# Kernel tuning notes

Measured on AMD Instinct MI355X. Metric: run time of the kernel, lower is better.

## Reference

```python
import jax, jax.numpy as jnp
import numpy as np

LOG2PI = float(np.log(2.0 * np.pi))


def setup_inputs() -> dict:
    key = jax.random.key(0)
    ks = jax.random.split(key, 5)
    B, T, XD, C = 128, 2050, 6, 64
    return {
        "x": jax.random.normal(ks[0], (B, T, XD), jnp.float32),
        "observation_means": jax.random.uniform(ks[1], (C, XD), dtype=jnp.float32),
        "observation_stddevs": jax.random.uniform(ks[2], (C, XD), dtype=jnp.float32),
        "log_A": jax.random.normal(ks[3], (C, C), jnp.float32),
        "log_pi": jax.random.normal(ks[4], (C,), jnp.float32),
    }


def _emission_logprob(x, means, stds):
    # Normal(means[:, :4], relu(stds[:, :4]) + 0.1).log_prob(x[:, :, :4]) summed over feat dim
    mu = means[:, :4]                       # (C,4)
    sigma = jax.nn.relu(stds[:, :4]) + 0.1  # (C,4)
    z = (x[:, :, None, :4] - mu) / sigma    # (B,T,C,4)
    return jnp.sum(-0.5 * z * z - jnp.log(sigma) - 0.5 * LOG2PI, axis=-1)  # (B,T,C)


def _forward_scalers(logp, log_A, log_pi):
    # scaled HMM forward pass; returns per-step log normalizers (T,B)
    a0 = logp[:, 0] + log_pi
    s0 = jax.nn.logsumexp(a0, axis=-1)
    a0n = a0 - s0[:, None]

    def step(a_prev, lp_t):
        a = lp_t + jax.nn.logsumexp(a_prev[:, :, None] + log_A[None], axis=1)
        s = jax.nn.logsumexp(a, axis=-1)
        return a - s[:, None], s

    _, s_rest = jax.lax.scan(step, a0n, jnp.swapaxes(logp[:, 1:], 0, 1))
    return jnp.concatenate([s0[None], s_rest], axis=0)  # (T,B)


def _viterbi(logp, log_A, log_pi):
    d0 = logp[:, 0] + log_pi  # (B,C)

    def step(d_prev, lp_t):
        scores = d_prev[:, :, None] + log_A[None]  # (B,C_prev,C_cur)
        psi_t = jnp.argmax(scores, axis=1)
        d = jnp.max(scores, axis=1) + lp_t
        return d, psi_t

    d_last, psi = jax.lax.scan(step, d0, jnp.swapaxes(logp[:, 1:], 0, 1))  # psi: (T-1,B,C)
    c_last = jnp.argmax(d_last, axis=-1)  # (B,)

    def back(c_next, psi_t):
        c_t = jnp.take_along_axis(psi_t, c_next[:, None], axis=1)[:, 0]
        return c_t, c_t

    _, cs = jax.lax.scan(back, c_last, psi, reverse=True)  # (T-1,B)
    c = jnp.concatenate([cs, c_last[None]], axis=0)  # (T,B)
    return jnp.swapaxes(c, 0, 1)  # (B,T)


def reference(x, observation_means, observation_stddevs, log_A, log_pi):
    logA = jax.nn.log_softmax(log_A, axis=1)
    logpi = jax.nn.log_softmax(log_pi, axis=0)
    logp = _emission_logprob(x, observation_means, observation_stddevs)  # (B,T,C)
    scalers = _forward_scalers(logp, logA, logpi)                         # (T,B)
    logp_x = jnp.sum(scalers, axis=0)                                     # (B,)
    c_est = _viterbi(logp, logA, logpi)                                   # (B,T) int
    return logp_x, c_est
```

## Files before the change

### kernel.cpp

```cpp
#include <hip/hip_runtime.h>

#define T_LEN 2050
#define B_SZ 128
#define NCHUNK 33
#define HL2PI 0.91893853320467274178f

__device__ __forceinline__ float waveMax(float v) {
#pragma unroll
    for (int off = 32; off >= 1; off >>= 1)
        v = fmaxf(v, __shfl_xor(v, off, 64));
    return v;
}
__device__ __forceinline__ float waveSum(float v) {
#pragma unroll
    for (int off = 32; off >= 1; off >>= 1)
        v += __shfl_xor(v, off, 64);
    return v;
}
__device__ __forceinline__ void waveArgmax(float& v, int& idx) {
#pragma unroll
    for (int off = 32; off >= 1; off >>= 1) {
        float ov = __shfl_xor(v, off, 64);
        int   oi = __shfl_xor(idx, off, 64);
        if (ov > v || (ov == v && oi < idx)) { v = ov; idx = oi; }
    }
}
__device__ __forceinline__ void cfence() { asm volatile("" ::: "memory"); }

__device__ __forceinline__ float rl(float v, int lane) {
    return __int_as_float(__builtin_amdgcn_readlane(__float_as_int(v), lane));
}

__device__ __forceinline__ float dppSumAll(float v) {
#define SSTEP(ctrl) { int t_ = __builtin_amdgcn_update_dpp(0, __float_as_int(v), ctrl, 0xf, 0xf, true); \
                      v = v + __int_as_float(t_); }
    SSTEP(0x111) SSTEP(0x112) SSTEP(0x114) SSTEP(0x118) SSTEP(0x142) SSTEP(0x143)
#undef SSTEP
    return __int_as_float(__builtin_amdgcn_readlane(__float_as_int(v), 63));
}
__device__ __forceinline__ float dppMaxAll(float v) {
#define MSTEP(ctrl) { int t_ = __builtin_amdgcn_update_dpp(__float_as_int(v), __float_as_int(v), ctrl, 0xf, 0xf, false); \
                      v = fmaxf(v, __int_as_float(t_)); }
    MSTEP(0x111) MSTEP(0x112) MSTEP(0x114) MSTEP(0x118) MSTEP(0x142) MSTEP(0x143)
#undef MSTEP
    return __int_as_float(__builtin_amdgcn_readlane(__float_as_int(v), 63));
}

extern "C" __global__ __launch_bounds__(64, 1)
void hmm_prep(const float* __restrict__ logA_in,
              const float* __restrict__ logpi_in,
              float* __restrict__ lAg,
              float* __restrict__ lpig)
{
    __shared__ float la[64 * 65];
    __shared__ float rowlse[64];
    const int j = threadIdx.x;
#pragma unroll
    for (int k = 0; k < 64; ++k)
        la[k * 65 + j] = logA_in[k * 64 + j];
    cfence();
    {
        float m = -1e30f;
#pragma unroll
        for (int k = 0; k < 64; ++k) m = fmaxf(m, la[j * 65 + k]);
        float s = 0.f;
#pragma unroll
        for (int k = 0; k < 64; ++k) s += expf(la[j * 65 + k] - m);
        rowlse[j] = m + logf(s);
    }
    cfence();
    {
        float v = logpi_in[j];
        float m = waveMax(v);
        float s = waveSum(expf(v - m));
        lpig[j] = v - (m + logf(s));
    }
    float4* o = (float4*)lAg;
#pragma unroll
    for (int k = 0; k < 16; ++k) {
        float4 v;
        v.x = la[(4 * k + 0) * 65 + j] - rowlse[4 * k + 0];
        v.y = la[(4 * k + 1) * 65 + j] - rowlse[4 * k + 1];
        v.z = la[(4 * k + 2) * 65 + j] - rowlse[4 * k + 2];
        v.w = la[(4 * k + 3) * 65 + j] - rowlse[4 * k + 3];
        o[j * 16 + k] = v;
    }
}

extern "C" __global__ __launch_bounds__(256)
void hmm_emis(const float* __restrict__ x,
              const float* __restrict__ means,
              const float* __restrict__ stds,
              float* __restrict__ buf,
              float* __restrict__ m_pre)
{
    const int wid = blockIdx.x * 4 + (threadIdx.x >> 6);
    const int j = threadIdx.x & 63;
    const int t = wid >> 7;
    const int b = wid & 127;

    const float* xt = x + ((size_t)b * T_LEN + t) * 6;
    float x0 = xt[0], x1 = xt[1], x2 = xt[2], x3 = xt[3];

    float mu0 = means[j * 6 + 0], mu1 = means[j * 6 + 1];
    float mu2 = means[j * 6 + 2], mu3 = means[j * 6 + 3];
    float sg0 = fmaxf(stds[j * 6 + 0], 0.f) + 0.1f;
    float sg1 = fmaxf(stds[j * 6 + 1], 0.f) + 0.1f;
    float sg2 = fmaxf(stds[j * 6 + 2], 0.f) + 0.1f;
    float sg3 = fmaxf(stds[j * 6 + 3], 0.f) + 0.1f;
    float ls0 = logf(sg0), ls1 = logf(sg1), ls2 = logf(sg2), ls3 = logf(sg3);

    float z0 = (x0 - mu0) / sg0, z1 = (x1 - mu1) / sg1;
    float z2 = (x2 - mu2) / sg2, z3 = (x3 - mu3) / sg3;
    float e0 = ((-0.5f * z0) * z0 - ls0) - HL2PI;
    float e1 = ((-0.5f * z1) * z1 - ls1) - HL2PI;
    float e2 = ((-0.5f * z2) * z2 - ls2) - HL2PI;
    float e3 = ((-0.5f * z3) * z3 - ls3) - HL2PI;
    float lp = ((e0 + e1) + e2) + e3;

    buf[((size_t)b * T_LEN + t) * 64 + j] = lp;
    float mm = waveMax(lp);
    if (j == 0) m_pre[(size_t)b * T_LEN + t] = mm;
}

extern "C" __global__ __launch_bounds__(64, 1)
void hmm_main(const float* __restrict__ x,
              const float* __restrict__ means,
              const float* __restrict__ stds,
              const float* __restrict__ lAg,
              const float* __restrict__ lpig,
              float* __restrict__ out,
              float* __restrict__ buf,
              const float* __restrict__ m_pre,
              int* __restrict__ c_last)
{
    __shared__ __align__(16) float xs[12304];

    const int j   = threadIdx.x;
    const int bid = blockIdx.x;
    const bool is_fwd = (bid < B_SZ);
    const int b = is_fwd ? bid : bid - B_SZ;

    float lpi = lpig[j];

    if (is_fwd) {
        {
            const float4* xg4 = (const float4*)(x + (size_t)b * T_LEN * 6);
            float4* xs4 = (float4*)xs;
            for (int i = j; i < 3075; i += 64) xs4[i] = xg4[i];
        }
        float mu0 = means[j * 6 + 0], mu1 = means[j * 6 + 1];
        float mu2 = means[j * 6 + 2], mu3 = means[j * 6 + 3];
        float sg0 = fmaxf(stds[j * 6 + 0], 0.f) + 0.1f;
        float sg1 = fmaxf(stds[j * 6 + 1], 0.f) + 0.1f;
        float sg2 = fmaxf(stds[j * 6 + 2], 0.f) + 0.1f;
        float sg3 = fmaxf(stds[j * 6 + 3], 0.f) + 0.1f;
        float ls0 = logf(sg0), ls1 = logf(sg1), ls2 = logf(sg2), ls3 = logf(sg3);
        float i0 = 1.f / sg0, i1 = 1.f / sg1, i2 = 1.f / sg2, i3 = 1.f / sg3;
        float cst = -(ls0 + ls1 + ls2 + ls3) - 4.f * HL2PI;

        float Ac[64];
        {
            const float4* g = (const float4*)lAg;
#pragma unroll
            for (int k = 0; k < 16; ++k) {
                float4 v = g[j * 16 + k];
                Ac[4 * k + 0] = __expf(v.x); Ac[4 * k + 1] = __expf(v.y);
                Ac[4 * k + 2] = __expf(v.z); Ac[4 * k + 3] = __expf(v.w);
            }
        }
        cfence();

        float z0 = (xs[0] - mu0) * i0, z1 = (xs[1] - mu1) * i1;
        float z2 = (xs[2] - mu2) * i2, z3 = (xs[3] - mu3) * i3;
        float a0 = (cst - 0.5f * (z0 * z0 + z1 * z1 + z2 * z2 + z3 * z3)) + lpi;
        float m0a = dppMaxAll(a0);
        float u = __expf(a0 - m0a);
        float s0 = dppSumAll(u);
        double acc = (double)(m0a + __logf(s0));
        u *= (1.0f / s0);

        const float* mp = m_pre + (size_t)b * T_LEN;
        float g0 = mp[1], g1 = mp[2], g2 = mp[3], g3 = mp[4];

#pragma unroll 1
        for (int t = 1; t < T_LEN; ++t) {
            float mm_c = g0; g0 = g1; g1 = g2; g2 = g3;
            int tp = t + 4; if (tp > T_LEN - 1) tp = T_LEN - 1;
            g3 = mp[tp];

            int o = t * 6;
            float y0 = xs[o], y1 = xs[o + 1], y2 = xs[o + 2], y3 = xs[o + 3];
            float w0 = (y0 - mu0) * i0, w1 = (y1 - mu1) * i1;
            float w2 = (y2 - mu2) * i2, w3 = (y3 - mu3) * i3;
            float lp = cst - 0.5f * (w0 * w0 + w1 * w1 + w2 * w2 + w3 * w3);
            float e_c = __expf(lp - mm_c);

            float q0 = 0.f, q1 = 0.f, q2 = 0.f, q3 = 0.f;
#pragma unroll
            for (int gq = 0; gq < 4; ++gq) {
                float s[16];
#pragma unroll
                for (int m = 0; m < 16; ++m) s[m] = rl(u, 16 * gq + m);
#pragma unroll
                for (int k2 = 0; k2 < 4; ++k2) {
                    const int i = 16 * gq + 4 * k2;
                    q0 = fmaf(s[4 * k2 + 0], Ac[i + 0], q0);
                    q1 = fmaf(s[4 * k2 + 1], Ac[i + 1], q1);
                    q2 = fmaf(s[4 * k2 + 2], Ac[i + 2], q2);
                    q3 = fmaf(s[4 * k2 + 3], Ac[i + 3], q3);
                }
            }
            u = ((q0 + q1) + (q2 + q3)) * e_c;
            acc += (double)mm_c;
            if ((t & 3) == 0) {
                float ss = dppSumAll(u);
                acc += (double)__logf(ss);
                u *= (1.0f / ss);
            }
        }
        float sf = dppSumAll(u);
        acc += (double)__logf(sf);
        if (j == 0) out[b] = (float)acc;
    } else {
        float lA[64];
        {
            const float4* g = (const float4*)lAg;
#pragma unroll
            for (int k = 0; k < 16; ++k) {
                float4 v = g[j * 16 + k];
                lA[4 * k + 0] = v.x; lA[4 * k + 1] = v.y;
                lA[4 * k + 2] = v.z; lA[4 * k + 3] = v.w;
            }
        }
        float* bb = buf + (size_t)b * T_LEN * 64 + j;

        float dn = bb[0] + lpi;
        float l0 = bb[64], l1 = bb[128], l2 = bb[192], l3 = bb[256];
        bb[0] = dn;

#pragma unroll 1
        for (int t = 1; t < T_LEN; ++t) {
            float lp_c = l0; l0 = l1; l1 = l2; l2 = l3;
            int tp = t + 4; if (tp > T_LEN - 1) tp = T_LEN - 1;
            l3 = bb[(size_t)tp * 64];

            float m0 = -3.4e38f, m1 = -3.4e38f, m2 = -3.4e38f, m3 = -3.4e38f;
#pragma unroll
            for (int gq = 0; gq < 4; ++gq) {
                float s[16];
#pragma unroll
                for (int m = 0; m < 16; ++m) s[m] = rl(dn, 16 * gq + m);
#pragma unroll
                for (int k2 = 0; k2 < 4; k2 += 2) {
                    const int ia = 16 * gq + 4 * k2;
                    const int ib = ia + 4;
                    float a0_ = s[4 * k2 + 0] + lA[ia + 0], b0_ = s[4 * k2 + 4] + lA[ib + 0];
                    float a1_ = s[4 * k2 + 1] + lA[ia + 1], b1_ = s[4 * k2 + 5] + lA[ib + 1];
                    float a2_ = s[4 * k2 + 2] + lA[ia + 2], b2_ = s[4 * k2 + 6] + lA[ib + 2];
                    float a3_ = s[4 * k2 + 3] + lA[ia + 3], b3_ = s[4 * k2 + 7] + lA[ib + 3];
                    m0 = fmaxf(fmaxf(m0, a0_), b0_);
                    m1 = fmaxf(fmaxf(m1, a1_), b1_);
                    m2 = fmaxf(fmaxf(m2, a2_), b2_);
                    m3 = fmaxf(fmaxf(m3, a3_), b3_);
                }
            }
            dn = fmaxf(fmaxf(m0, m1), fmaxf(m2, m3)) + lp_c;

            bb[(size_t)t * 64] = dn;
        }

        float vv = dn; int idx = j;
        waveArgmax(vv, idx);
        if (j == 0) c_last[b] = idx;
    }
}

extern "C" __global__ __launch_bounds__(256)
void hmm_psi(const float* __restrict__ buf,
             const float* __restrict__ lAg,
             unsigned char* __restrict__ psi)
{
    __shared__ __align__(16) float sd[4][64];
    const int warp = threadIdx.x >> 6;
    const int j = threadIdx.x & 63;
    const int wid = blockIdx.x * 4 + warp;

    float lA[64];
    {
        const float4* g = (const float4*)lAg;
#pragma unroll
        for (int k = 0; k < 16; ++k) {
            float4 v = g[j * 16 + k];
            lA[4 * k + 0] = v.x; lA[4 * k + 1] = v.y;
            lA[4 * k + 2] = v.z; lA[4 * k + 3] = v.w;
        }
    }
    const float4* dv = (const float4*)sd[warp];
    const int NP = 2049 * B_SZ;

    for (int p = wid; p < NP; p += 8192) {
        const int t = (p >> 7) + 1;
        const int b = p & 127;
        float dval = buf[((size_t)b * T_LEN + (t - 1)) * 64 + j];
        sd[warp][j] = dval;

        float bv0 = -3.4e38f, bv1 = -3.4e38f, bv2 = -3.4e38f, bv3 = -3.4e38f;
        int bi0 = 0, bi1 = 1, bi2 = 2, bi3 = 3;
#pragma unroll
        for (int k = 0; k < 16; ++k) {
            float4 dd = dv[k];
            float v0 = dd.x + lA[4 * k + 0];
            float v1 = dd.y + lA[4 * k + 1];
            float v2 = dd.z + lA[4 * k + 2];
            float v3 = dd.w + lA[4 * k + 3];
            if (v0 > bv0) { bv0 = v0; bi0 = 4 * k + 0; }
            if (v1 > bv1) { bv1 = v1; bi1 = 4 * k + 1; }
            if (v2 > bv2) { bv2 = v2; bi2 = 4 * k + 2; }
            if (v3 > bv3) { bv3 = v3; bi3 = 4 * k + 3; }
        }
        float best = bv0; int bidx = bi0;
        if (bv1 > best || (bv1 == best && bi1 < bidx)) { best = bv1; bidx = bi1; }
        if (bv2 > best || (bv2 == best && bi2 < bidx)) { best = bv2; bidx = bi2; }
        if (bv3 > best || (bv3 == best && bi3 < bidx)) { best = bv3; bidx = bi3; }

        psi[((size_t)t * B_SZ + b) * 64 + j] = (unsigned char)bidx;
    }
}

extern "C" __global__ __launch_bounds__(256)
void hmm_compose(const unsigned char* __restrict__ psi,
                 unsigned char* __restrict__ mt)
{
    const int w = blockIdx.x * 4 + (threadIdx.x >> 6);
    const int j = threadIdx.x & 63;
    const int g = w % NCHUNK;
    const int b = w / NCHUNK;
    const int e = (g < NCHUNK - 1) ? g * 64 + 64 : (T_LEN - 1);
    int M = j;
    for (int t = e; t >= g * 64 + 1; --t)
        M = psi[((size_t)t * B_SZ + b) * 64 + M];
    mt[((size_t)g * B_SZ + b) * 64 + j] = (unsigned char)M;
}

extern "C" __global__ __launch_bounds__(64, 1)
void hmm_fill(const unsigned char* __restrict__ psi,
              const unsigned char* __restrict__ mt,
              const int* __restrict__ c_last,
              float* __restrict__ out)
{
    __shared__ int sb[NCHUNK];
    const int b = blockIdx.x;
    const int g = threadIdx.x;
    const int cl = c_last[b];
    if (g == 0) {
        int cur = cl;
        for (int q = NCHUNK - 1; q >= 0; --q) {
            cur = mt[((size_t)q * B_SZ + b) * 64 + cur];
            sb[q] = cur;
        }
    }
    cfence();
    float* oc = out + B_SZ + (size_t)b * T_LEN;
    if (g == NCHUNK) {
        oc[T_LEN - 1] = (float)cl;
    } else if (g < NCHUNK) {
        const int e = (g < NCHUNK - 1) ? g * 64 + 64 : (T_LEN - 1);
        int s = (g < NCHUNK - 1) ? sb[g + 1] : cl;
        for (int t = e; t >= g * 64 + 1; --t) {
            s = psi[((size_t)t * B_SZ + b) * 64 + s];
            oc[t - 1] = (float)s;
        }
    }
}

extern "C" void kernel_launch(void* const* d_in, const int* in_sizes, int n_in,
                              void* d_out, int out_size, void* d_ws, size_t ws_size,
                              hipStream_t stream)
{
    const float* x      = (const float*)d_in[0];
    const float* means  = (const float*)d_in[1];
    const float* stds   = (const float*)d_in[2];
    const float* logA   = (const float*)d_in[3];
    const float* logpi  = (const float*)d_in[4];
    float* out = (float*)d_out;

    char* base = (char*)d_ws;
    float*         buf   = (float*)base;
    unsigned char* psi   = (unsigned char*)(base + 67174400);
    float*         m_pre = (float*)(base + 67174400);
    unsigned char* mt    = (unsigned char*)(base + 83968000);
    int*           cl    = (int*)(base + 84238336);
    float*         lAg   = (float*)(base + 84238848);
    float*         lpig  = (float*)(base + 84255232);

    hipLaunchKernelGGL(hmm_prep, dim3(1), dim3(64), 0, stream, logA, logpi, lAg, lpig);
    hipLaunchKernelGGL(hmm_emis, dim3((T_LEN * B_SZ) / 4), dim3(256), 0, stream,
                       x, means, stds, buf, m_pre);
    hipLaunchKernelGGL(hmm_main, dim3(2 * B_SZ), dim3(64), 0, stream,
                       x, means, stds, lAg, lpig, out, buf, m_pre, cl);
    hipLaunchKernelGGL(hmm_psi, dim3(2048), dim3(256), 0, stream, buf, lAg, psi);
    hipLaunchKernelGGL(hmm_compose, dim3((NCHUNK * B_SZ) / 4), dim3(256), 0, stream, psi, mt);
    hipLaunchKernelGGL(hmm_fill, dim3(B_SZ), dim3(64), 0, stream, psi, mt, cl, out);
}
```

Measured before the change: 1.015 ms.

## Stream x and max-prefix through registers per 64-step chunk instead of LDS staging

The forward path no longer copies the whole x sequence into shared memory. Each lane instead loads one timestep's features and max value per 64-step chunk, prefetches the next chunk, and broadcasts them across lanes with readlane. The loop is unrolled by four so renormalisation happens without a branch test, and sched_barriers are added to the readlane/FMA reductions. The Viterbi loop is split so the clamped prefetch index disappears. This removes the LDS staging prologue and the per-step LDS reads, but adds readlane traffic on the serial critical path.

```diff
diff --git a/kernel.cpp b/kernel.cpp
--- a/kernel.cpp
+++ b/kernel.cpp
@@ -122,6 +122,66 @@
     float mm = waveMax(lp);
     if (j == 0) m_pre[(size_t)b * T_LEN + t] = mm;
 }
+
+#define FWD_REDUCE(SRC)                                                   \
+    float q0 = 0.f, q1 = 0.f, q2 = 0.f, q3 = 0.f;                         \
+    _Pragma("unroll")                                                     \
+    for (int gq = 0; gq < 4; ++gq) {                                      \
+        float s_[16];                                                     \
+        _Pragma("unroll")                                                 \
+        for (int m_ = 0; m_ < 16; ++m_) s_[m_] = rl((SRC), 16 * gq + m_); \
+        __builtin_amdgcn_sched_barrier(0);                                \
+        _Pragma("unroll")                                                 \
+        for (int k2 = 0; k2 < 4; ++k2) {                                  \
+            const int i_ = 16 * gq + 4 * k2;                              \
+            q0 = fmaf(s_[4 * k2 + 0], Ac[i_ + 0], q0);                    \
+            q1 = fmaf(s_[4 * k2 + 1], Ac[i_ + 1], q1);                    \
+            q2 = fmaf(s_[4 * k2 + 2], Ac[i_ + 2], q2);                    \
+            q3 = fmaf(s_[4 * k2 + 3], Ac[i_ + 3], q3);                    \
+        }                                                                 \
+    }
+
+#define FSTEP(LI, RN) {                                                   \
+    const int l_ = l + (LI);                                              \
+    float mm_c = rl(mA, l_);                                              \
+    float y0 = rl(xA0, l_), y1 = rl(xA1, l_);                             \
+    float y2 = rl(xA2, l_), y3 = rl(xA3, l_);                             \
+    float w0 = (y0 - mu0) * i0, w1 = (y1 - mu1) * i1;                     \
+    float w2 = (y2 - mu2) * i2, w3 = (y3 - mu3) * i3;                     \
+    float lp = cst - 0.5f * (w0 * w0 + w1 * w1 + w2 * w2 + w3 * w3);      \
+    float e_c = __expf(lp - mm_c);                                        \
+    FWD_REDUCE(u);                                                        \
+    u = ((q0 + q1) + (q2 + q3)) * e_c;                                    \
+    acc += (double)mm_c;                                                  \
+    if (RN) {                                                             \
+        float ss = dppSumAll(u);                                          \
+        acc += (double)__logf(ss);                                        \
+        u *= (1.0f / ss);                                                 \
+    }                                                                     \
+}
+
+#define VIT_REDUCE(SRC)                                                   \
+    float m0 = -3.4e38f, m1 = -3.4e38f, m2 = -3.4e38f, m3 = -3.4e38f;     \
+    _Pragma("unroll")                                                     \
+    for (int gq = 0; gq < 4; ++gq) {                                      \
+        float s_[16];                                                     \
+        _Pragma("unroll")                                                 \
+        for (int m_ = 0; m_ < 16; ++m_) s_[m_] = rl((SRC), 16 * gq + m_); \
+        __builtin_amdgcn_sched_barrier(0);                                \
+        _Pragma("unroll")                                                 \
+        for (int k2 = 0; k2 < 4; k2 += 2) {                               \
+            const int ia = 16 * gq + 4 * k2;                              \
+            const int ib = ia + 4;                                        \
+            float a0_ = s_[4*k2+0] + lA[ia+0], b0_ = s_[4*k2+4] + lA[ib+0]; \
+            float a1_ = s_[4*k2+1] + lA[ia+1], b1_ = s_[4*k2+5] + lA[ib+1]; \
+            float a2_ = s_[4*k2+2] + lA[ia+2], b2_ = s_[4*k2+6] + lA[ib+2]; \
+            float a3_ = s_[4*k2+3] + lA[ia+3], b3_ = s_[4*k2+7] + lA[ib+3]; \
+            m0 = fmaxf(fmaxf(m0, a0_), b0_);                              \
+            m1 = fmaxf(fmaxf(m1, a1_), b1_);                              \
+            m2 = fmaxf(fmaxf(m2, a2_), b2_);                              \
+            m3 = fmaxf(fmaxf(m3, a3_), b3_);                              \
+        }                                                                 \
+    }
 
 extern "C" __global__ __launch_bounds__(64, 1)
 void hmm_main(const float* __restrict__ x,
@@ -134,8 +194,6 @@
               const float* __restrict__ m_pre,
               int* __restrict__ c_last)
 {
-    __shared__ __align__(16) float xs[12304];
-
     const int j   = threadIdx.x;
     const int bid = blockIdx.x;
     const bool is_fwd = (bid < B_SZ);
@@ -144,11 +202,9 @@
     float lpi = lpig[j];
 
     if (is_fwd) {
-        {
-            const float4* xg4 = (const float4*)(x + (size_t)b * T_LEN * 6);
-            float4* xs4 = (float4*)xs;
-            for (int i = j; i < 3075; i += 64) xs4[i] = xg4[i];
-        }
+        const float* xb = x + (size_t)b * T_LEN * 6;
+        const float* mp = m_pre + (size_t)b * T_LEN;
+
         float mu0 = means[j * 6 + 0], mu1 = means[j * 6 + 1];
         float mu2 = means[j * 6 + 2], mu3 = means[j * 6 + 3];
         float sg0 = fmaxf(stds[j * 6 + 0], 0.f) + 0.1f;
@@ -169,10 +225,9 @@
                 Ac[4 * k + 2] = __expf(v.z); Ac[4 * k + 3] = __expf(v.w);
             }
         }
-        cfence();
-
-        float z0 = (xs[0] - mu0) * i0, z1 = (xs[1] - mu1) * i1;
-        float z2 = (xs[2] - mu2) * i2, z3 = (xs[3] - mu3) * i3;
+
+        float z0 = (xb[0] - mu0) * i0, z1 = (xb[1] - mu1) * i1;
+        float z2 = (xb[2] - mu2) * i2, z3 = (xb[3] - mu3) * i3;
         float a0 = (cst - 0.5f * (z0 * z0 + z1 * z1 + z2 * z2 + z3 * z3)) + lpi;
         float m0a = dppMaxAll(a0);
         float u = __expf(a0 - m0a);
@@ -180,44 +235,39 @@
         double acc = (double)(m0a + __logf(s0));
         u *= (1.0f / s0);
 
-        const float* mp = m_pre + (size_t)b * T_LEN;
-        float g0 = mp[1], g1 = mp[2], g2 = mp[3], g3 = mp[4];
+        float xA0, xA1, xA2, xA3, mA;
+        {
+            const float* p = xb + (size_t)(1 + j) * 6;
+            xA0 = p[0]; xA1 = p[1]; xA2 = p[2]; xA3 = p[3];
+            mA = mp[1 + j];
+        }
+        float xB0 = 0.f, xB1 = 0.f, xB2 = 0.f, xB3 = 0.f, mB = 0.f;
 
 #pragma unroll 1
-        for (int t = 1; t < T_LEN; ++t) {
-            float mm_c = g0; g0 = g1; g1 = g2; g2 = g3;
-            int tp = t + 4; if (tp > T_LEN - 1) tp = T_LEN - 1;
-            g3 = mp[tp];
-
-            int o = t * 6;
-            float y0 = xs[o], y1 = xs[o + 1], y2 = xs[o + 2], y3 = xs[o + 3];
+        for (int c = 0; c < 32; ++c) {
+            if (c < 31) {
+                const int idx = 65 + 64 * c + j;
+                const float* p = xb + (size_t)idx * 6;
+                xB0 = p[0]; xB1 = p[1]; xB2 = p[2]; xB3 = p[3];
+                mB = mp[idx];
+            }
+#pragma unroll 1
+            for (int l = 0; l < 64; l += 4) {
+                FSTEP(0, false) FSTEP(1, false) FSTEP(2, false) FSTEP(3, true)
+            }
+            xA0 = xB0; xA1 = xB1; xA2 = xB2; xA3 = xB3; mA = mB;
+        }
+        {
+            const float* p = xb + (size_t)2049 * 6;
+            float y0 = p[0], y1 = p[1], y2 = p[2], y3 = p[3];
+            float mm_c = mp[2049];
             float w0 = (y0 - mu0) * i0, w1 = (y1 - mu1) * i1;
             float w2 = (y2 - mu2) * i2, w3 = (y3 - mu3) * i3;
             float lp = cst - 0.5f * (w0 * w0 + w1 * w1 + w2 * w2 + w3 * w3);
             float e_c = __expf(lp - mm_c);
-
-            float q0 = 0.f, q1 = 0.f, q2 = 0.f, q3 = 0.f;
-#pragma unroll
-            for (int gq = 0; gq < 4; ++gq) {
-                float s[16];
-#pragma unroll
-                for (int m = 0; m < 16; ++m) s[m] = rl(u, 16 * gq + m);
-#pragma unroll
-                for (int k2 = 0; k2 < 4; ++k2) {
-                    const int i = 16 * gq + 4 * k2;
-                    q0 = fmaf(s[4 * k2 + 0], Ac[i + 0], q0);
-                    q1 = fmaf(s[4 * k2 + 1], Ac[i + 1], q1);
-                    q2 = fmaf(s[4 * k2 + 2], Ac[i + 2], q2);
-                    q3 = fmaf(s[4 * k2 + 3], Ac[i + 3], q3);
-                }
-            }
+            FWD_REDUCE(u);
             u = ((q0 + q1) + (q2 + q3)) * e_c;
             acc += (double)mm_c;
-            if ((t & 3) == 0) {
-                float ss = dppSumAll(u);
-                acc += (double)__logf(ss);
-                u *= (1.0f / ss);
-            }
         }
         float sf = dppSumAll(u);
         acc += (double)__logf(sf);
@@ -240,33 +290,18 @@
         bb[0] = dn;
 
 #pragma unroll 1
-        for (int t = 1; t < T_LEN; ++t) {
+        for (int t = 1; t <= T_LEN - 5; ++t) {
             float lp_c = l0; l0 = l1; l1 = l2; l2 = l3;
-            int tp = t + 4; if (tp > T_LEN - 1) tp = T_LEN - 1;
-            l3 = bb[(size_t)tp * 64];
-
-            float m0 = -3.4e38f, m1 = -3.4e38f, m2 = -3.4e38f, m3 = -3.4e38f;
-#pragma unroll
-            for (int gq = 0; gq < 4; ++gq) {
-                float s[16];
-#pragma unroll
-                for (int m = 0; m < 16; ++m) s[m] = rl(dn, 16 * gq + m);
-#pragma unroll
-                for (int k2 = 0; k2 < 4; k2 += 2) {
-                    const int ia = 16 * gq + 4 * k2;
-                    const int ib = ia + 4;
-                    float a0_ = s[4 * k2 + 0] + lA[ia + 0], b0_ = s[4 * k2 + 4] + lA[ib + 0];
-                    float a1_ = s[4 * k2 + 1] + lA[ia + 1], b1_ = s[4 * k2 + 5] + lA[ib + 1];
-                    float a2_ = s[4 * k2 + 2] + lA[ia + 2], b2_ = s[4 * k2 + 6] + lA[ib + 2];
-                    float a3_ = s[4 * k2 + 3] + lA[ia + 3], b3_ = s[4 * k2 + 7] + lA[ib + 3];
-                    m0 = fmaxf(fmaxf(m0, a0_), b0_);
-                    m1 = fmaxf(fmaxf(m1, a1_), b1_);
-                    m2 = fmaxf(fmaxf(m2, a2_), b2_);
-                    m3 = fmaxf(fmaxf(m3, a3_), b3_);
-                }
-            }
+            l3 = bb[(size_t)(t + 4) * 64];
+            VIT_REDUCE(dn);
             dn = fmaxf(fmaxf(m0, m1), fmaxf(m2, m3)) + lp_c;
-
+            bb[(size_t)t * 64] = dn;
+        }
+#pragma unroll 1
+        for (int t = T_LEN - 4; t < T_LEN; ++t) {
+            float lp_c = l0; l0 = l1; l1 = l2; l2 = l3;
+            VIT_REDUCE(dn);
+            dn = fmaxf(fmaxf(m0, m1), fmaxf(m2, m3)) + lp_c;
             bb[(size_t)t * 64] = dn;
         }
 
```

Result: no change. 1.033 ms (+1.8%).
